# Kernel tuning notes

Hardware: AMD Instinct MI355X
Metric: run time of the kernel (lower is better)

## Reference

```python
import jax, jax.numpy as jnp
import numpy as np

N_NODES = 50000
N_EDGES = 800000
IN_DIM = 128
HID_DIM = 64
OUT_DIM = 64
NUM_GRAPHS = 512


def setup_inputs() -> dict:
    key = jax.random.key(0)
    ks = jax.random.split(key, 8)
    x = jax.random.normal(ks[0], (N_NODES, IN_DIM), dtype=jnp.float32)
    edge_index = jax.random.randint(ks[1], (2, N_EDGES), 0, N_NODES, dtype=jnp.int64)
    batch = jnp.sort(jax.random.randint(ks[2], (N_NODES,), 0, NUM_GRAPHS, dtype=jnp.int64))
    s1 = 1.0 / np.sqrt(IN_DIM)
    s2 = 1.0 / np.sqrt(HID_DIM)
    W1 = jax.random.uniform(ks[3], (IN_DIM, HID_DIM), jnp.float32, -s1, s1)
    b1 = jax.random.uniform(ks[4], (HID_DIM,), jnp.float32, -s1, s1)
    W2 = jax.random.uniform(ks[5], (HID_DIM, OUT_DIM), jnp.float32, -s2, s2)
    b2 = jax.random.uniform(ks[6], (OUT_DIM,), jnp.float32, -s2, s2)
    return {"x": x, "edge_index": edge_index, "batch": batch,
            "W1": W1, "b1": b1, "W2": W2, "b2": b2}


def _gcn_layer(h, W, b, src, dst, norm, n_nodes):
    # linear transform first (keeps the per-edge gather at output width)
    h = h @ W + b                      # [N, d_out]
    msg = h[src] * norm[:, None]       # [E, d_out] gathered, normalized messages
    agg = jax.ops.segment_sum(msg, dst, num_segments=n_nodes)  # scatter-add
    return jax.nn.relu(agg)


def reference(x, edge_index, batch, W1, b1, W2, b2):
    src, dst = edge_index[0], edge_index[1]
    # symmetric degree normalization: deg^{-1/2}[src] * deg^{-1/2}[dst]
    deg = jax.ops.segment_sum(jnp.ones((src.shape[0],), x.dtype), dst,
                              num_segments=N_NODES)
    dinv = jax.lax.rsqrt(jnp.maximum(deg, 1.0))
    norm = dinv[src] * dinv[dst]       # [E]

    h = _gcn_layer(x, W1, b1, src, dst, norm, N_NODES)   # dropout = identity (eval)
    h = _gcn_layer(h, W2, b2, src, dst, norm, N_NODES)

    # scatter_mean pooling over batch indices
    sums = jax.ops.segment_sum(h, batch, num_segments=NUM_GRAPHS)
    cnts = jax.ops.segment_sum(jnp.ones((N_NODES,), h.dtype), batch,
                               num_segments=NUM_GRAPHS)
    return sums / jnp.maximum(cnts, 1.0)[:, None]        # [NUM_GRAPHS, OUT_DIM]
```

## Files before the change

kernel.cpp:

```cpp
#include <hip/hip_runtime.h>
#include <hip/hip_fp16.h>

#define N_NODES 50000
#define N_EDGES 800000
#define IN_DIM 128
#define NUM_GRAPHS 512
#define CAP 64
#define NB 392
#define BCAP 2816
#define FILL_T 2048
#define NFILL 391
#define GEMM1_BLKS 391
#define AGG_BLKS 391

typedef unsigned short u16;
typedef unsigned int u32;

__device__ __forceinline__ void acc_row(const uint4& v, float2& aa, float2& ab,
                                        float2& ac, float2& ad) {
    const __half2* hp = reinterpret_cast<const __half2*>(&v);
    float2 f;
    f = __half22float2(hp[0]); aa.x += f.x; aa.y += f.y;
    f = __half22float2(hp[1]); ab.x += f.x; ab.y += f.y;
    f = __half22float2(hp[2]); ac.x += f.x; ac.y += f.y;
    f = __half22float2(hp[3]); ad.x += f.x; ad.y += f.y;
}

__device__ __forceinline__ void acc_row_s(const uint4& v, float dv, float2& aa,
                                          float2& ab, float2& ac, float2& ad) {
    const __half2* hp = reinterpret_cast<const __half2*>(&v);
    float2 f;
    f = __half22float2(hp[0]); aa.x = fmaf(f.x, dv, aa.x); aa.y = fmaf(f.y, dv, aa.y);
    f = __half22float2(hp[1]); ab.x = fmaf(f.x, dv, ab.x); ab.y = fmaf(f.y, dv, ab.y);
    f = __half22float2(hp[2]); ac.x = fmaf(f.x, dv, ac.x); ac.y = fmaf(f.y, dv, ac.y);
    f = __half22float2(hp[3]); ad.x = fmaf(f.x, dv, ad.x); ad.y = fmaf(f.y, dv, ad.y);
}

__device__ __forceinline__ void gather_node(
    const uint4* __restrict__ H16, const u16* __restrict__ sp, int dg, int lo,
    float2& aa, float2& ab, float2& ac, float2& ad) {
    int i = 0;
    for (; i + 7 < dg; i += 8) {
        ushort4 s4a = *reinterpret_cast<const ushort4*>(sp + i);
        ushort4 s4b = *reinterpret_cast<const ushort4*>(sp + i + 4);
        uint4 v0 = H16[(size_t)s4a.x * 8 + lo];
        uint4 v1 = H16[(size_t)s4a.y * 8 + lo];
        uint4 v2 = H16[(size_t)s4a.z * 8 + lo];
        uint4 v3 = H16[(size_t)s4a.w * 8 + lo];
        uint4 v4 = H16[(size_t)s4b.x * 8 + lo];
        uint4 v5 = H16[(size_t)s4b.y * 8 + lo];
        uint4 v6 = H16[(size_t)s4b.z * 8 + lo];
        uint4 v7 = H16[(size_t)s4b.w * 8 + lo];
        acc_row(v0, aa, ab, ac, ad); acc_row(v1, aa, ab, ac, ad);
        acc_row(v2, aa, ab, ac, ad); acc_row(v3, aa, ab, ac, ad);
        acc_row(v4, aa, ab, ac, ad); acc_row(v5, aa, ab, ac, ad);
        acc_row(v6, aa, ab, ac, ad); acc_row(v7, aa, ab, ac, ad);
    }
    for (; i + 3 < dg; i += 4) {
        ushort4 s4 = *reinterpret_cast<const ushort4*>(sp + i);
        uint4 v0 = H16[(size_t)s4.x * 8 + lo];
        uint4 v1 = H16[(size_t)s4.y * 8 + lo];
        uint4 v2 = H16[(size_t)s4.z * 8 + lo];
        uint4 v3 = H16[(size_t)s4.w * 8 + lo];
        acc_row(v0, aa, ab, ac, ad); acc_row(v1, aa, ab, ac, ad);
        acc_row(v2, aa, ab, ac, ad); acc_row(v3, aa, ab, ac, ad);
    }
    for (; i < dg; ++i) {
        uint4 v = H16[(size_t)sp[i] * 8 + lo];
        acc_row(v, aa, ab, ac, ad);
    }
}

__device__ __forceinline__ void gather_node_s(
    const uint4* __restrict__ H16, const u16* __restrict__ sp,
    const float* __restrict__ dinv, int dg, int lo,
    float2& aa, float2& ab, float2& ac, float2& ad) {
    int i = 0;
    for (; i + 7 < dg; i += 8) {
        ushort4 s4a = *reinterpret_cast<const ushort4*>(sp + i);
        ushort4 s4b = *reinterpret_cast<const ushort4*>(sp + i + 4);
        uint4 v0 = H16[(size_t)s4a.x * 8 + lo];
        uint4 v1 = H16[(size_t)s4a.y * 8 + lo];
        uint4 v2 = H16[(size_t)s4a.z * 8 + lo];
        uint4 v3 = H16[(size_t)s4a.w * 8 + lo];
        uint4 v4 = H16[(size_t)s4b.x * 8 + lo];
        uint4 v5 = H16[(size_t)s4b.y * 8 + lo];
        uint4 v6 = H16[(size_t)s4b.z * 8 + lo];
        uint4 v7 = H16[(size_t)s4b.w * 8 + lo];
        float d0 = dinv[s4a.x], d1 = dinv[s4a.y], d2 = dinv[s4a.z], d3 = dinv[s4a.w];
        float d4 = dinv[s4b.x], d5 = dinv[s4b.y], d6 = dinv[s4b.z], d7 = dinv[s4b.w];
        acc_row_s(v0, d0, aa, ab, ac, ad); acc_row_s(v1, d1, aa, ab, ac, ad);
        acc_row_s(v2, d2, aa, ab, ac, ad); acc_row_s(v3, d3, aa, ab, ac, ad);
        acc_row_s(v4, d4, aa, ab, ac, ad); acc_row_s(v5, d5, aa, ab, ac, ad);
        acc_row_s(v6, d6, aa, ab, ac, ad); acc_row_s(v7, d7, aa, ab, ac, ad);
    }
    for (; i + 3 < dg; i += 4) {
        ushort4 s4 = *reinterpret_cast<const ushort4*>(sp + i);
        uint4 v0 = H16[(size_t)s4.x * 8 + lo];
        uint4 v1 = H16[(size_t)s4.y * 8 + lo];
        uint4 v2 = H16[(size_t)s4.z * 8 + lo];
        uint4 v3 = H16[(size_t)s4.w * 8 + lo];
        float d0 = dinv[s4.x], d1 = dinv[s4.y], d2 = dinv[s4.z], d3 = dinv[s4.w];
        acc_row_s(v0, d0, aa, ab, ac, ad); acc_row_s(v1, d1, aa, ab, ac, ad);
        acc_row_s(v2, d2, aa, ab, ac, ad); acc_row_s(v3, d3, aa, ab, ac, ad);
    }
    for (; i < dg; ++i) {
        uint4 v = H16[(size_t)sp[i] * 8 + lo];
        float dv = dinv[sp[i]];
        acc_row_s(v, dv, aa, ab, ac, ad);
    }
}

__global__ __launch_bounds__(256) void gemm1_fill_kernel(
    const float* __restrict__ X, const float* __restrict__ W,
    const float* __restrict__ bias, __half* __restrict__ Yh, int n_nodes,
    const int* __restrict__ src, const int* __restrict__ dst,
    int* __restrict__ gcursor, u32* __restrict__ packed, int n_edges) {
    __shared__ float xst[32][128];
    __shared__ float ws[32][64];
    __shared__ int cnt2[NB], goffs[NB];
    const int tid = threadIdx.x;

    if (blockIdx.x & 1) {
        const int fb = blockIdx.x >> 1;
        for (int i = tid; i < NB; i += 256) cnt2[i] = 0;
        __syncthreads();
        const int base = fb * FILL_T;
        int d[8], s[8], pl[8];
#pragma unroll
        for (int i = 0; i < 8; ++i) {
            int e = base + i * 256 + tid;
            if (e < n_edges) {
                d[i] = dst[e]; s[i] = src[e];
                pl[i] = atomicAdd(&cnt2[d[i] >> 7], 1);
            } else d[i] = -1;
        }
        __syncthreads();
        for (int b = tid; b < NB; b += 256)
            if (cnt2[b] > 0) goffs[b] = atomicAdd(&gcursor[b], cnt2[b]);
        __syncthreads();
#pragma unroll
        for (int i = 0; i < 8; ++i) {
            if (d[i] >= 0) {
                int b = d[i] >> 7;
                packed[(size_t)b * BCAP + goffs[b] + pl[i]] =
                    ((u32)d[i] << 16) | (u32)s[i];
            }
        }
        return;
    }

    const int idx = blockIdx.x >> 1;
    if (idx >= GEMM1_BLKS) return;
    const int base = idx * 128;
    const int lane = tid & 63;
    const int w = tid >> 6;
    const int jo = lane & 7;
    const int rg = lane >> 3;
    const int rowb = w * 32 + rg * 4;

    float cc[4][8];
    {
        float4 ba = *reinterpret_cast<const float4*>(bias + jo * 8);
        float4 bb = *reinterpret_cast<const float4*>(bias + jo * 8 + 4);
#pragma unroll
        for (int r = 0; r < 4; ++r) {
            cc[r][0] = ba.x; cc[r][1] = ba.y; cc[r][2] = ba.z; cc[r][3] = ba.w;
            cc[r][4] = bb.x; cc[r][5] = bb.y; cc[r][6] = bb.z; cc[r][7] = bb.w;
        }
    }
    const float4* X4 = reinterpret_cast<const float4*>(X);
    const float4* W4 = reinterpret_cast<const float4*>(W);
    float4* ws4 = reinterpret_cast<float4*>(&ws[0][0]);

    for (int kc = 0; kc < 4; ++kc) {
        if (kc) __syncthreads();
#pragma unroll
        for (int t = 0; t < 4; ++t) {
            int i = t * 256 + tid;
            int row = i >> 3, f4 = i & 7;
            float4 v = make_float4(0.f, 0.f, 0.f, 0.f);
            if (base + row < n_nodes) v = X4[(size_t)(base + row) * 32 + kc * 8 + f4];
            int k0 = f4 * 4;
            xst[k0 + 0][row] = v.x; xst[k0 + 1][row] = v.y;
            xst[k0 + 2][row] = v.z; xst[k0 + 3][row] = v.w;
        }
#pragma unroll
        for (int t = 0; t < 2; ++t)
            ws4[t * 256 + tid] = W4[kc * 512 + t * 256 + tid];
        __syncthreads();

#pragma unroll 8
        for (int kk = 0; kk < 32; ++kk) {
            float4 xv = *reinterpret_cast<const float4*>(&xst[kk][rowb]);
            float4 wa = *reinterpret_cast<const float4*>(&ws[kk][jo * 8]);
            float4 wb = *reinterpret_cast<const float4*>(&ws[kk][jo * 8 + 4]);
            float xr[4] = {xv.x, xv.y, xv.z, xv.w};
            float wv[8] = {wa.x, wa.y, wa.z, wa.w, wb.x, wb.y, wb.z, wb.w};
#pragma unroll
            for (int r = 0; r < 4; ++r)
#pragma unroll
                for (int j = 0; j < 8; ++j) cc[r][j] += xr[r] * wv[j];
        }
    }

#pragma unroll
    for (int r = 0; r < 4; ++r) {
        int row = base + rowb + r;
        if (row < n_nodes) {
            __half2 h0 = __floats2half2_rn(cc[r][0], cc[r][1]);
            __half2 h1 = __floats2half2_rn(cc[r][2], cc[r][3]);
            __half2 h2 = __floats2half2_rn(cc[r][4], cc[r][5]);
            __half2 h3 = __floats2half2_rn(cc[r][6], cc[r][7]);
            uint4 o;
            o.x = *reinterpret_cast<u32*>(&h0); o.y = *reinterpret_cast<u32*>(&h1);
            o.z = *reinterpret_cast<u32*>(&h2); o.w = *reinterpret_cast<u32*>(&h3);
            *reinterpret_cast<uint4*>(Yh + (size_t)row * 64 + jo * 8) = o;
        }
    }
}

__global__ __launch_bounds__(256) void fine_kernel(
    const u32* __restrict__ packed, const int* __restrict__ gcursor,
    u16* __restrict__ ssorted, int* __restrict__ deg, float* __restrict__ dinv,
    const int* __restrict__ batch, int* __restrict__ gstart, int n_graphs) {
    __shared__ u16 image[128 * CAP];
    __shared__ int cur[128];
    const int tid = threadIdx.x;

    if (blockIdx.x == NB) {
        for (int g = tid; g <= n_graphs; g += 256) {
            int lo = 0, hi = N_NODES;
            while (lo < hi) {
                int mid = (lo + hi) >> 1;
                if (batch[mid] < g) lo = mid + 1; else hi = mid;
            }
            gstart[g] = lo;
        }
        return;
    }

    const int b = blockIdx.x;
    if (tid < 128) cur[tid] = 0;
    __syncthreads();
    const int cnt = gcursor[b];
    const u32* pp = packed + (size_t)b * BCAP;
    for (int i = tid; i < cnt; i += 256) {
        u32 p = pp[i];
        int loc = (p >> 16) & 127;
        int pos = atomicAdd(&cur[loc], 1);
        if (pos < CAP) image[loc * CAP + pos] = (u16)(p & 0xffff);
    }
    __syncthreads();
    const int nbase = b * 128;
    if (tid < 128) {
        int c = cur[tid];
        int d = nbase + tid;
        if (d < N_NODES) {
            deg[d] = c;
            dinv[d] = rsqrtf(fmaxf((float)c, 1.0f));
        }
    }
    __syncthreads();
    const u32* im32 = reinterpret_cast<const u32*>(image);
    u32* out32 = reinterpret_cast<u32*>(ssorted) + (size_t)nbase * (CAP / 2);
    for (int i = tid; i < 128 * CAP / 2; i += 256) out32[i] = im32[i];
}

__global__ __launch_bounds__(256) void agg_gemm_kernel(
    const __half* __restrict__ H, const u16* __restrict__ ssorted,
    const int* __restrict__ deg, const float* __restrict__ dinv,
    const float* __restrict__ W, const float* __restrict__ bias,
    __half* __restrict__ Yh, int n_nodes) {
    __shared__ float xs[128][68];
    __shared__ float ws[64][64];
    const int tid = threadIdx.x;
    const int lane = tid & 63;
    const int w = tid >> 6;
    const int lo = lane & 7;
    const int grp = tid >> 3;
    const int base = blockIdx.x * 128;
    const uint4* H16 = reinterpret_cast<const uint4*>(H);

    {
        const float4* W4 = reinterpret_cast<const float4*>(W);
        float4* ws4 = reinterpret_cast<float4*>(&ws[0][0]);
#pragma unroll
        for (int t = 0; t < 4; ++t) ws4[t * 256 + tid] = W4[t * 256 + tid];
    }

    for (int t = 0; t < 4; ++t) {
        int slot = grp + 32 * t;
        int node = base + slot;
        float2 aa = make_float2(0.f, 0.f), ab = make_float2(0.f, 0.f);
        float2 ac = make_float2(0.f, 0.f), ad = make_float2(0.f, 0.f);
        float dv = 0.f;
        if (node < n_nodes) {
            int dg = min(deg[node], CAP);
            gather_node_s(H16, ssorted + (size_t)node * CAP, dinv, dg, lo,
                          aa, ab, ac, ad);
            dv = dinv[node];
        }
        *reinterpret_cast<float4*>(&xs[slot][8 * lo]) =
            make_float4(fmaxf(aa.x * dv, 0.f), fmaxf(aa.y * dv, 0.f),
                        fmaxf(ab.x * dv, 0.f), fmaxf(ab.y * dv, 0.f));
        *reinterpret_cast<float4*>(&xs[slot][8 * lo + 4]) =
            make_float4(fmaxf(ac.x * dv, 0.f), fmaxf(ac.y * dv, 0.f),
                        fmaxf(ad.x * dv, 0.f), fmaxf(ad.y * dv, 0.f));
    }
    __syncthreads();

    const int half = w >> 1;
    const int rg = lane >> 3;
    const int c0 = (w & 1) * 32 + lo * 4;
    float cc[8][4];
    {
        float4 bv = *reinterpret_cast<const float4*>(bias + c0);
#pragma unroll
        for (int i = 0; i < 8; ++i) {
            cc[i][0] = bv.x; cc[i][1] = bv.y; cc[i][2] = bv.z; cc[i][3] = bv.w;
        }
    }
#pragma unroll 4
    for (int k = 0; k < 64; k += 4) {
        float4 xv[8];
#pragma unroll
        for (int i = 0; i < 8; ++i)
            xv[i] = *reinterpret_cast<const float4*>(&xs[half * 64 + rg + 8 * i][k]);
        float wr[4][4];
#pragma unroll
        for (int j = 0; j < 4; ++j) {
            float4 wv = *reinterpret_cast<const float4*>(&ws[k + j][c0]);
            wr[j][0] = wv.x; wr[j][1] = wv.y; wr[j][2] = wv.z; wr[j][3] = wv.w;
        }
#pragma unroll
        for (int i = 0; i < 8; ++i) {
            float xr[4] = {xv[i].x, xv[i].y, xv[i].z, xv[i].w};
#pragma unroll
            for (int kk = 0; kk < 4; ++kk)
#pragma unroll
                for (int j = 0; j < 4; ++j)
                    cc[i][j] = fmaf(xr[kk], wr[kk][j], cc[i][j]);
        }
    }

#pragma unroll
    for (int i = 0; i < 8; ++i) {
        int row = base + half * 64 + rg + 8 * i;
        if (row < n_nodes) {
            float dv = dinv[row];
            __half2 h0 = __floats2half2_rn(cc[i][0] * dv, cc[i][1] * dv);
            __half2 h1 = __floats2half2_rn(cc[i][2] * dv, cc[i][3] * dv);
            uint2 o;
            o.x = *reinterpret_cast<u32*>(&h0);
            o.y = *reinterpret_cast<u32*>(&h1);
            *reinterpret_cast<uint2*>(Yh + (size_t)row * 64 + c0) = o;
        }
    }
}

__global__ __launch_bounds__(512) void agg2_pool_kernel(
    const __half* __restrict__ H, const u16* __restrict__ ssorted,
    const int* __restrict__ deg, const float* __restrict__ dinv,
    const int* __restrict__ gstart, float* __restrict__ out) {
    __shared__ float part[64][64];
    const int g = blockIdx.x;
    const int tid = threadIdx.x;
    const int lane = tid & 63;
    const int w = tid >> 6;
    const int lo = lane & 7;
    const int slot = w * 8 + (lane >> 3);
    const uint4* H16 = reinterpret_cast<const uint4*>(H);
    const int beg = gstart[g], end = gstart[g + 1];

    float2 pa = make_float2(0.f, 0.f), pb = make_float2(0.f, 0.f);
    float2 pc = make_float2(0.f, 0.f), pd = make_float2(0.f, 0.f);
    for (int node = beg + slot; node < end; node += 64) {
        int dg = min(deg[node], CAP);
        float2 aa = make_float2(0.f, 0.f), ab = make_float2(0.f, 0.f);
        float2 ac = make_float2(0.f, 0.f), ad = make_float2(0.f, 0.f);
        gather_node(H16, ssorted + (size_t)node * CAP, dg, lo, aa, ab, ac, ad);
        float dv = dinv[node];
        pa.x += fmaxf(aa.x * dv, 0.f); pa.y += fmaxf(aa.y * dv, 0.f);
        pb.x += fmaxf(ab.x * dv, 0.f); pb.y += fmaxf(ab.y * dv, 0.f);
        pc.x += fmaxf(ac.x * dv, 0.f); pc.y += fmaxf(ac.y * dv, 0.f);
        pd.x += fmaxf(ad.x * dv, 0.f); pd.y += fmaxf(ad.y * dv, 0.f);
    }
    *reinterpret_cast<float4*>(&part[slot][8 * lo]) = make_float4(pa.x, pa.y, pb.x, pb.y);
    *reinterpret_cast<float4*>(&part[slot][8 * lo + 4]) = make_float4(pc.x, pc.y, pd.x, pd.y);
    __syncthreads();
    if (tid < 64) {
        float s = 0.f;
#pragma unroll
        for (int r = 0; r < 64; ++r) s += part[r][tid];
        out[(size_t)g * 64 + tid] = s / fmaxf((float)(end - beg), 1.0f);
    }
}

extern "C" void kernel_launch(void* const* d_in, const int* in_sizes, int n_in,
                              void* d_out, int out_size, void* d_ws, size_t ws_size,
                              hipStream_t stream) {
    const float* x     = (const float*)d_in[0];
    const int*   ei    = (const int*)d_in[1];
    const int*   batch = (const int*)d_in[2];
    const float* W1    = (const float*)d_in[3];
    const float* b1    = (const float*)d_in[4];
    const float* W2    = (const float*)d_in[5];
    const float* b2    = (const float*)d_in[6];
    float* out = (float*)d_out;

    const int* srcp = ei;
    const int* dstp = ei + N_EDGES;

    __half* H1h     = (__half*)d_ws;
    __half* H2h     = H1h + (size_t)N_NODES * 64;
    float*  dinv    = (float*)(H2h + (size_t)N_NODES * 64);
    int*    deg     = (int*)(dinv + N_NODES);
    u16*    ssorted = (u16*)(deg + N_NODES);
    u32*    packed  = (u32*)(ssorted + (size_t)NB * 128 * CAP);
    int*    gcursor = (int*)(packed + (size_t)NB * BCAP);
    int*    gstart  = gcursor + NB;

    hipMemsetAsync(gcursor, 0, NB * sizeof(int), stream);

    gemm1_fill_kernel<<<2 * NFILL, 256, 0, stream>>>(
        x, W1, b1, H1h, N_NODES, srcp, dstp, gcursor, packed, N_EDGES);

    fine_kernel<<<NB + 1, 256, 0, stream>>>(
        packed, gcursor, ssorted, deg, dinv, batch, gstart, NUM_GRAPHS);

    agg_gemm_kernel<<<AGG_BLKS, 256, 0, stream>>>(
        H1h, ssorted, deg, dinv, W2, b2, H2h, N_NODES);

    agg2_pool_kernel<<<NUM_GRAPHS, 512, 0, stream>>>(
        H2h, ssorted, deg, dinv, gstart, out);
}
```

Before: 172.9 us.

## Fuse per-bucket CSR sort into layer-2 aggregation+GEMM and compute degrees atomically

Merges the fine sort kernel with the aggregation+GEMM kernel, so each block builds its bucket's sorted neighbor list in LDS and gathers from there instead of re-reading it from global memory. Degrees are now counted with global atomics during the edge-fill pass, and dinv is recomputed on the fly with rsqrt rather than stored. The gstart binary search moves into the first kernel and W2 is read from global memory instead of being staged in LDS. This removes one launch and a round trip through the sorted index buffer, in exchange for extra global atomics on degree and more rsqrt work per gathered edge.

New measurement: 178.5 us. +3.3%, slower.

```diff
diff --git a/kernel.cpp b/kernel.cpp
--- a/kernel.cpp
+++ b/kernel.cpp
@@ -11,10 +11,19 @@
 #define FILL_T 2048
 #define NFILL 391
 #define GEMM1_BLKS 391
-#define AGG_BLKS 391
 
 typedef unsigned short u16;
 typedef unsigned int u32;
+
+__device__ __forceinline__ void acc_row_s(const uint4& v, float dv, float2& aa,
+                                          float2& ab, float2& ac, float2& ad) {
+    const __half2* hp = reinterpret_cast<const __half2*>(&v);
+    float2 f;
+    f = __half22float2(hp[0]); aa.x = fmaf(f.x, dv, aa.x); aa.y = fmaf(f.y, dv, aa.y);
+    f = __half22float2(hp[1]); ab.x = fmaf(f.x, dv, ab.x); ab.y = fmaf(f.y, dv, ab.y);
+    f = __half22float2(hp[2]); ac.x = fmaf(f.x, dv, ac.x); ac.y = fmaf(f.y, dv, ac.y);
+    f = __half22float2(hp[3]); ad.x = fmaf(f.x, dv, ad.x); ad.y = fmaf(f.y, dv, ad.y);
+}
 
 __device__ __forceinline__ void acc_row(const uint4& v, float2& aa, float2& ab,
                                         float2& ac, float2& ad) {
@@ -26,14 +35,49 @@
     f = __half22float2(hp[3]); ad.x += f.x; ad.y += f.y;
 }
 
-__device__ __forceinline__ void acc_row_s(const uint4& v, float dv, float2& aa,
-                                          float2& ab, float2& ac, float2& ad) {
-    const __half2* hp = reinterpret_cast<const __half2*>(&v);
-    float2 f;
-    f = __half22float2(hp[0]); aa.x = fmaf(f.x, dv, aa.x); aa.y = fmaf(f.y, dv, aa.y);
-    f = __half22float2(hp[1]); ab.x = fmaf(f.x, dv, ab.x); ab.y = fmaf(f.y, dv, ab.y);
-    f = __half22float2(hp[2]); ac.x = fmaf(f.x, dv, ac.x); ac.y = fmaf(f.y, dv, ac.y);
-    f = __half22float2(hp[3]); ad.x = fmaf(f.x, dv, ad.x); ad.y = fmaf(f.y, dv, ad.y);
+__device__ __forceinline__ float deg_dinv(const int* __restrict__ deg, int s) {
+    return rsqrtf(fmaxf((float)deg[s], 1.0f));
+}
+
+__device__ __forceinline__ void gather_lds_s(
+    const uint4* __restrict__ H16, const u16* sp, const int* __restrict__ deg,
+    int dg, int lo, float2& aa, float2& ab, float2& ac, float2& ad) {
+    int i = 0;
+    for (; i + 7 < dg; i += 8) {
+        ushort4 s4a = *reinterpret_cast<const ushort4*>(sp + i);
+        ushort4 s4b = *reinterpret_cast<const ushort4*>(sp + i + 4);
+        uint4 v0 = H16[(size_t)s4a.x * 8 + lo];
+        uint4 v1 = H16[(size_t)s4a.y * 8 + lo];
+        uint4 v2 = H16[(size_t)s4a.z * 8 + lo];
+        uint4 v3 = H16[(size_t)s4a.w * 8 + lo];
+        uint4 v4 = H16[(size_t)s4b.x * 8 + lo];
+        uint4 v5 = H16[(size_t)s4b.y * 8 + lo];
+        uint4 v6 = H16[(size_t)s4b.z * 8 + lo];
+        uint4 v7 = H16[(size_t)s4b.w * 8 + lo];
+        float d0 = deg_dinv(deg, s4a.x), d1 = deg_dinv(deg, s4a.y);
+        float d2 = deg_dinv(deg, s4a.z), d3 = deg_dinv(deg, s4a.w);
+        float d4 = deg_dinv(deg, s4b.x), d5 = deg_dinv(deg, s4b.y);
+        float d6 = deg_dinv(deg, s4b.z), d7 = deg_dinv(deg, s4b.w);
+        acc_row_s(v0, d0, aa, ab, ac, ad); acc_row_s(v1, d1, aa, ab, ac, ad);
+        acc_row_s(v2, d2, aa, ab, ac, ad); acc_row_s(v3, d3, aa, ab, ac, ad);
+        acc_row_s(v4, d4, aa, ab, ac, ad); acc_row_s(v5, d5, aa, ab, ac, ad);
+        acc_row_s(v6, d6, aa, ab, ac, ad); acc_row_s(v7, d7, aa, ab, ac, ad);
+    }
+    for (; i + 3 < dg; i += 4) {
+        ushort4 s4 = *reinterpret_cast<const ushort4*>(sp + i);
+        uint4 v0 = H16[(size_t)s4.x * 8 + lo];
+        uint4 v1 = H16[(size_t)s4.y * 8 + lo];
+        uint4 v2 = H16[(size_t)s4.z * 8 + lo];
+        uint4 v3 = H16[(size_t)s4.w * 8 + lo];
+        float d0 = deg_dinv(deg, s4.x), d1 = deg_dinv(deg, s4.y);
+        float d2 = deg_dinv(deg, s4.z), d3 = deg_dinv(deg, s4.w);
+        acc_row_s(v0, d0, aa, ab, ac, ad); acc_row_s(v1, d1, aa, ab, ac, ad);
+        acc_row_s(v2, d2, aa, ab, ac, ad); acc_row_s(v3, d3, aa, ab, ac, ad);
+    }
+    for (; i < dg; ++i) {
+        uint4 v = H16[(size_t)sp[i] * 8 + lo];
+        acc_row_s(v, deg_dinv(deg, sp[i]), aa, ab, ac, ad);
+    }
 }
 
 __device__ __forceinline__ void gather_node(
@@ -71,55 +115,29 @@
     }
 }
 
-__device__ __forceinline__ void gather_node_s(
-    const uint4* __restrict__ H16, const u16* __restrict__ sp,
-    const float* __restrict__ dinv, int dg, int lo,
-    float2& aa, float2& ab, float2& ac, float2& ad) {
-    int i = 0;
-    for (; i + 7 < dg; i += 8) {
-        ushort4 s4a = *reinterpret_cast<const ushort4*>(sp + i);
-        ushort4 s4b = *reinterpret_cast<const ushort4*>(sp + i + 4);
-        uint4 v0 = H16[(size_t)s4a.x * 8 + lo];
-        uint4 v1 = H16[(size_t)s4a.y * 8 + lo];
-        uint4 v2 = H16[(size_t)s4a.z * 8 + lo];
-        uint4 v3 = H16[(size_t)s4a.w * 8 + lo];
-        uint4 v4 = H16[(size_t)s4b.x * 8 + lo];
-        uint4 v5 = H16[(size_t)s4b.y * 8 + lo];
-        uint4 v6 = H16[(size_t)s4b.z * 8 + lo];
-        uint4 v7 = H16[(size_t)s4b.w * 8 + lo];
-        float d0 = dinv[s4a.x], d1 = dinv[s4a.y], d2 = dinv[s4a.z], d3 = dinv[s4a.w];
-        float d4 = dinv[s4b.x], d5 = dinv[s4b.y], d6 = dinv[s4b.z], d7 = dinv[s4b.w];
-        acc_row_s(v0, d0, aa, ab, ac, ad); acc_row_s(v1, d1, aa, ab, ac, ad);
-        acc_row_s(v2, d2, aa, ab, ac, ad); acc_row_s(v3, d3, aa, ab, ac, ad);
-        acc_row_s(v4, d4, aa, ab, ac, ad); acc_row_s(v5, d5, aa, ab, ac, ad);
-        acc_row_s(v6, d6, aa, ab, ac, ad); acc_row_s(v7, d7, aa, ab, ac, ad);
-    }
-    for (; i + 3 < dg; i += 4) {
-        ushort4 s4 = *reinterpret_cast<const ushort4*>(sp + i);
-        uint4 v0 = H16[(size_t)s4.x * 8 + lo];
-        uint4 v1 = H16[(size_t)s4.y * 8 + lo];
-        uint4 v2 = H16[(size_t)s4.z * 8 + lo];
-        uint4 v3 = H16[(size_t)s4.w * 8 + lo];
-        float d0 = dinv[s4.x], d1 = dinv[s4.y], d2 = dinv[s4.z], d3 = dinv[s4.w];
-        acc_row_s(v0, d0, aa, ab, ac, ad); acc_row_s(v1, d1, aa, ab, ac, ad);
-        acc_row_s(v2, d2, aa, ab, ac, ad); acc_row_s(v3, d3, aa, ab, ac, ad);
-    }
-    for (; i < dg; ++i) {
-        uint4 v = H16[(size_t)sp[i] * 8 + lo];
-        float dv = dinv[sp[i]];
-        acc_row_s(v, dv, aa, ab, ac, ad);
-    }
-}
-
 __global__ __launch_bounds__(256) void gemm1_fill_kernel(
     const float* __restrict__ X, const float* __restrict__ W,
-    const float* __restrict__ bias, __half* __restrict__ Yh, int n_nodes,
+    const float* __restrict__ bias, __half* __restrict__ Yh,
     const int* __restrict__ src, const int* __restrict__ dst,
-    int* __restrict__ gcursor, u32* __restrict__ packed, int n_edges) {
+    int* __restrict__ deg, int* __restrict__ gcursor,
+    u32* __restrict__ packed,
+    const int* __restrict__ batch, int* __restrict__ gstart) {
     __shared__ float xst[32][128];
     __shared__ float ws[32][64];
     __shared__ int cnt2[NB], goffs[NB];
     const int tid = threadIdx.x;
+
+    if (blockIdx.x == 2 * NFILL) {
+        for (int g = tid; g <= NUM_GRAPHS; g += 256) {
+            int lo = 0, hi = N_NODES;
+            while (lo < hi) {
+                int mid = (lo + hi) >> 1;
+                if (batch[mid] < g) lo = mid + 1; else hi = mid;
+            }
+            gstart[g] = lo;
+        }
+        return;
+    }
 
     if (blockIdx.x & 1) {
         const int fb = blockIdx.x >> 1;
@@ -130,9 +148,10 @@
 #pragma unroll
         for (int i = 0; i < 8; ++i) {
             int e = base + i * 256 + tid;
-            if (e < n_edges) {
+            if (e < N_EDGES) {
                 d[i] = dst[e]; s[i] = src[e];
                 pl[i] = atomicAdd(&cnt2[d[i] >> 7], 1);
+                atomicAdd(&deg[d[i]], 1);
             } else d[i] = -1;
         }
         __syncthreads();
@@ -151,7 +170,6 @@
     }
 
     const int idx = blockIdx.x >> 1;
-    if (idx >= GEMM1_BLKS) return;
     const int base = idx * 128;
     const int lane = tid & 63;
     const int w = tid >> 6;
@@ -180,7 +198,7 @@
             int i = t * 256 + tid;
             int row = i >> 3, f4 = i & 7;
             float4 v = make_float4(0.f, 0.f, 0.f, 0.f);
-            if (base + row < n_nodes) v = X4[(size_t)(base + row) * 32 + kc * 8 + f4];
+            if (base + row < N_NODES) v = X4[(size_t)(base + row) * 32 + kc * 8 + f4];
             int k0 = f4 * 4;
             xst[k0 + 0][row] = v.x; xst[k0 + 1][row] = v.y;
             xst[k0 + 2][row] = v.z; xst[k0 + 3][row] = v.w;
@@ -207,7 +225,7 @@
 #pragma unroll
     for (int r = 0; r < 4; ++r) {
         int row = base + rowb + r;
-        if (row < n_nodes) {
+        if (row < N_NODES) {
             __half2 h0 = __floats2half2_rn(cc[r][0], cc[r][1]);
             __half2 h1 = __floats2half2_rn(cc[r][2], cc[r][3]);
             __half2 h2 = __floats2half2_rn(cc[r][4], cc[r][5]);
@@ -220,27 +238,17 @@
     }
 }
 
-__global__ __launch_bounds__(256) void fine_kernel(
+__global__ __launch_bounds__(256) void sort_agg_kernel(
     const u32* __restrict__ packed, const int* __restrict__ gcursor,
-    u16* __restrict__ ssorted, int* __restrict__ deg, float* __restrict__ dinv,
-    const int* __restrict__ batch, int* __restrict__ gstart, int n_graphs) {
+    const int* __restrict__ deg, u16* __restrict__ ssorted,
+    const __half* __restrict__ H, const float* __restrict__ W,
+    const float* __restrict__ bias, __half* __restrict__ Yh) {
     __shared__ u16 image[128 * CAP];
     __shared__ int cur[128];
+    __shared__ float xs[128][68];
     const int tid = threadIdx.x;
-
-    if (blockIdx.x == NB) {
-        for (int g = tid; g <= n_graphs; g += 256) {
-            int lo = 0, hi = N_NODES;
-            while (lo < hi) {
-                int mid = (lo + hi) >> 1;
-                if (batch[mid] < g) lo = mid + 1; else hi = mid;
-            }
-            gstart[g] = lo;
-        }
-        return;
-    }
-
     const int b = blockIdx.x;
+
     if (tid < 128) cur[tid] = 0;
     __syncthreads();
     const int cnt = gcursor[b];
@@ -252,54 +260,30 @@
         if (pos < CAP) image[loc * CAP + pos] = (u16)(p & 0xffff);
     }
     __syncthreads();
+
     const int nbase = b * 128;
-    if (tid < 128) {
-        int c = cur[tid];
-        int d = nbase + tid;
-        if (d < N_NODES) {
-            deg[d] = c;
-            dinv[d] = rsqrtf(fmaxf((float)c, 1.0f));
-        }
-    }
-    __syncthreads();
-    const u32* im32 = reinterpret_cast<const u32*>(image);
-    u32* out32 = reinterpret_cast<u32*>(ssorted) + (size_t)nbase * (CAP / 2);
-    for (int i = tid; i < 128 * CAP / 2; i += 256) out32[i] = im32[i];
-}
-
-__global__ __launch_bounds__(256) void agg_gemm_kernel(
-    const __half* __restrict__ H, const u16* __restrict__ ssorted,
-    const int* __restrict__ deg, const float* __restrict__ dinv,
-    const float* __restrict__ W, const float* __restrict__ bias,
-    __half* __restrict__ Yh, int n_nodes) {
-    __shared__ float xs[128][68];
-    __shared__ float ws[64][64];
-    const int tid = threadIdx.x;
+    {
+        const u32* im32 = reinterpret_cast<const u32*>(image);
+        u32* out32 = reinterpret_cast<u32*>(ssorted) + (size_t)nbase * (CAP / 2);
+        for (int i = tid; i < 128 * CAP / 2; i += 256) out32[i] = im32[i];
+    }
+
     const int lane = tid & 63;
     const int w = tid >> 6;
     const int lo = lane & 7;
     const int grp = tid >> 3;
-    const int base = blockIdx.x * 128;
     const uint4* H16 = reinterpret_cast<const uint4*>(H);
-
-    {
-        const float4* W4 = reinterpret_cast<const float4*>(W);
-        float4* ws4 = reinterpret_cast<float4*>(&ws[0][0]);
-#pragma unroll
-        for (int t = 0; t < 4; ++t) ws4[t * 256 + tid] = W4[t * 256 + tid];
-    }
-
     for (int t = 0; t < 4; ++t) {
         int slot = grp + 32 * t;
-        int node = base + slot;
+        int node = nbase + slot;
         float2 aa = make_float2(0.f, 0.f), ab = make_float2(0.f, 0.f);
         float2 ac = make_float2(0.f, 0.f), ad = make_float2(0.f, 0.f);
         float dv = 0.f;
-        if (node < n_nodes) {
-            int dg = min(deg[node], CAP);
-            gather_node_s(H16, ssorted + (size_t)node * CAP, dinv, dg, lo,
-                          aa, ab, ac, ad);
-            dv = dinv[node];
+        if (node < N_NODES) {
+            int c = cur[slot];
+            int dg = min(c, CAP);
+            gather_lds_s(H16, image + slot * CAP, deg, dg, lo, aa, ab, ac, ad);
+            dv = rsqrtf(fmaxf((float)c, 1.0f));
         }
         *reinterpret_cast<float4*>(&xs[slot][8 * lo]) =
             make_float4(fmaxf(aa.x * dv, 0.f), fmaxf(aa.y * dv, 0.f),
@@ -313,6 +297,8 @@
     const int half = w >> 1;
     const int rg = lane >> 3;
     const int c0 = (w & 1) * 32 + lo * 4;
+    const float4* Wg = reinterpret_cast<const float4*>(W);
+    const int wcol = (w & 1) * 8 + lo;
     float cc[8][4];
     {
         float4 bv = *reinterpret_cast<const float4*>(bias + c0);
@@ -330,7 +316,7 @@
         float wr[4][4];
 #pragma unroll
         for (int j = 0; j < 4; ++j) {
-            float4 wv = *reinterpret_cast<const float4*>(&ws[k + j][c0]);
+            float4 wv = Wg[(k + j) * 16 + wcol];
             wr[j][0] = wv.x; wr[j][1] = wv.y; wr[j][2] = wv.z; wr[j][3] = wv.w;
         }
 #pragma unroll
@@ -346,9 +332,10 @@
 
 #pragma unroll
     for (int i = 0; i < 8; ++i) {
-        int row = base + half * 64 + rg + 8 * i;
-        if (row < n_nodes) {
-            float dv = dinv[row];
+        int slot = half * 64 + rg + 8 * i;
+        int row = nbase + slot;
+        if (row < N_NODES) {
+            float dv = rsqrtf(fmaxf((float)cur[slot], 1.0f));
             __half2 h0 = __floats2half2_rn(cc[i][0] * dv, cc[i][1] * dv);
             __half2 h1 = __floats2half2_rn(cc[i][2] * dv, cc[i][3] * dv);
             uint2 o;
@@ -361,8 +348,8 @@
 
 __global__ __launch_bounds__(512) void agg2_pool_kernel(
     const __half* __restrict__ H, const u16* __restrict__ ssorted,
-    const int* __restrict__ deg, const float* __restrict__ dinv,
-    const int* __restrict__ gstart, float* __restrict__ out) {
+    const int* __restrict__ deg, const int* __restrict__ gstart,
+    float* __restrict__ out) {
     __shared__ float part[64][64];
     const int g = blockIdx.x;
     const int tid = threadIdx.x;
@@ -376,11 +363,11 @@
     float2 pa = make_float2(0.f, 0.f), pb = make_float2(0.f, 0.f);
     float2 pc = make_float2(0.f, 0.f), pd = make_float2(0.f, 0.f);
     for (int node = beg + slot; node < end; node += 64) {
-        int dg = min(deg[node], CAP);
+        int dgv = min(deg[node], CAP);
         float2 aa = make_float2(0.f, 0.f), ab = make_float2(0.f, 0.f);
         float2 ac = make_float2(0.f, 0.f), ad = make_float2(0.f, 0.f);
-        gather_node(H16, ssorted + (size_t)node * CAP, dg, lo, aa, ab, ac, ad);
-        float dv = dinv[node];
+        gather_node(H16, ssorted + (size_t)node * CAP, dgv, lo, aa, ab, ac, ad);
+        float dv = rsqrtf(fmaxf((float)deg[node], 1.0f));
         pa.x += fmaxf(aa.x * dv, 0.f); pa.y += fmaxf(aa.y * dv, 0.f);
         pb.x += fmaxf(ab.x * dv, 0.f); pb.y += fmaxf(ab.y * dv, 0.f);
         pc.x += fmaxf(ac.x * dv, 0.f); pc.y += fmaxf(ac.y * dv, 0.f);
@@ -414,24 +401,20 @@
 
     __half* H1h     = (__half*)d_ws;
     __half* H2h     = H1h + (size_t)N_NODES * 64;
-    float*  dinv    = (float*)(H2h + (size_t)N_NODES * 64);
-    int*    deg     = (int*)(dinv + N_NODES);
-    u16*    ssorted = (u16*)(deg + N_NODES);
+    u16*    ssorted = (u16*)(H2h + (size_t)N_NODES * 64);
     u32*    packed  = (u32*)(ssorted + (size_t)NB * 128 * CAP);
-    int*    gcursor = (int*)(packed + (size_t)NB * BCAP);
+    int*    deg     = (int*)(packed + (size_t)NB * BCAP);
+    int*    gcursor = deg + N_NODES;
     int*    gstart  = gcursor + NB;
 
-    hipMemsetAsync(gcursor, 0, NB * sizeof(int), stream);
-
-    gemm1_fill_kernel<<<2 * NFILL, 256, 0, stream>>>(
-        x, W1, b1, H1h, N_NODES, srcp, dstp, gcursor, packed, N_EDGES);
-
-    fine_kernel<<<NB + 1, 256, 0, stream>>>(
-        packed, gcursor, ssorted, deg, dinv, batch, gstart, NUM_GRAPHS);
-
-    agg_gemm_kernel<<<AGG_BLKS, 256, 0, stream>>>(
-        H1h, ssorted, deg, dinv, W2, b2, H2h, N_NODES);
+    hipMemsetAsync(deg, 0, (N_NODES + NB) * sizeof(int), stream);
+
+    gemm1_fill_kernel<<<2 * NFILL + 1, 256, 0, stream>>>(
+        x, W1, b1, H1h, srcp, dstp, deg, gcursor, packed, batch, gstart);
+
+    sort_agg_kernel<<<NB, 256, 0, stream>>>(
+        packed, gcursor, deg, ssorted, H1h, W2, b2, H2h);
 
     agg2_pool_kernel<<<NUM_GRAPHS, 512, 0, stream>>>(
-        H2h, ssorted, deg, dinv, gstart, out);
-}
+        H2h, ssorted, deg, gstart, out);
+}
```
